# Kernel tuning notes

Measured on AMD Instinct MI355X. Metric: run time of the kernel, lower is better.

The kernel has to match this reference:

```python
import jax, jax.numpy as jnp
import numpy as np

N, D_IN = 8192, 1024
FC1, FC2, FC3 = 256, 128, 64
DQK = FC3 // 8  # 8


def setup_inputs() -> dict:
    key = jax.random.key(0)
    ks = jax.random.split(key, 20)
    s = 0.05
    inp = {
        "x": jax.random.normal(ks[0], (N, D_IN), jnp.float32),
        # feature extractor MLP (dropout omitted: eval mode)
        "W1": jax.random.normal(ks[1], (D_IN, FC1), jnp.float32) * s,
        "b1": jnp.zeros((FC1,), jnp.float32),
        "W2": jax.random.normal(ks[2], (FC1, FC2), jnp.float32) * s,
        "b2": jnp.zeros((FC2,), jnp.float32),
        "W3": jax.random.normal(ks[3], (FC2, FC3), jnp.float32) * s,
        "b3": jnp.zeros((FC3,), jnp.float32),
        # 1x1 conv Q/K/V == linear layers on the 64-dim embedding
        "Wq": jax.random.normal(ks[4], (FC3, DQK), jnp.float32) * s,
        "bq": jnp.zeros((DQK,), jnp.float32),
        "Wk": jax.random.normal(ks[5], (FC3, DQK), jnp.float32) * s,
        "bk": jnp.zeros((DQK,), jnp.float32),
        "Wv": jax.random.normal(ks[6], (FC3, FC3), jnp.float32) * s,
        "bv": jnp.zeros((FC3,), jnp.float32),
        "gamma": jnp.array([0.5], jnp.float32),  # learned residual scale (init 0 in torch)
        # attention-pooling branch
        "Wa1": jax.random.normal(ks[7], (FC3, FC3), jnp.float32) * s,
        "ba1": jnp.zeros((FC3,), jnp.float32),
        "Wa2": jax.random.normal(ks[8], (FC3, 1), jnp.float32) * s,
        "ba2": jnp.zeros((1,), jnp.float32),
        # classifier
        "Wc": jax.random.normal(ks[9], (FC3, 1), jnp.float32) * s,
        "bc": jnp.zeros((1,), jnp.float32),
    }
    return inp


def reference(x, W1, b1, W2, b2, W3, b3, Wq, bq, Wk, bk, Wv, bv, gamma,
              Wa1, ba1, Wa2, ba2, Wc, bc):
    # instance feature extractor (dropout identity at eval)
    H = jax.nn.relu(x @ W1 + b1)
    H = jax.nn.relu(H @ W2 + b2)
    H = jax.nn.relu(H @ W3 + b3)                 # [N, 64]
    # self-attention over instances (unscaled dot product)
    Q = H @ Wq + bq                              # [N, 8]
    K = H @ Wk + bk                              # [N, 8]
    V = H @ Wv + bv                              # [N, 64]
    att = jax.nn.softmax(Q @ K.T, axis=-1)       # [N, N] full score matrix
    H = gamma[0] * (att @ V) + H                 # residual scale-add
    # attention-based MIL pooling
    scores = jnp.tanh(H @ Wa1 + ba1) @ Wa2 + ba2 # [N, 1]
    A = jax.nn.softmax(scores[:, 0])             # [N]
    M = A @ H                                    # [64] bag embedding
    Y = jax.nn.sigmoid(M @ Wc + bc)[0]
    Y_prob = jnp.clip(Y, 1e-5, 1.0 - 1e-5)
    return (Y_prob, M)
```

## Files before the change

kernel.cpp:

```cpp
#include <hip/hip_runtime.h>
#include <math.h>

typedef unsigned short ushort_t;
typedef __attribute__((ext_vector_type(8))) short short8;
typedef __attribute__((ext_vector_type(4))) float f32x4;

__device__ inline unsigned bfpair(float lo, float hi) {
  unsigned r;
  asm("v_cvt_pk_bf16_f32 %0, %1, %2" : "=v"(r) : "v"(lo), "v"(hi));
  return r;
}
__device__ inline ushort_t bf16of(float v) { return (ushort_t)(bfpair(v, v) & 0xffffu); }
__device__ inline void permswap32(unsigned &a, unsigned &b) {
  asm("v_permlane32_swap_b32 %0, %1" : "+v"(a), "+v"(b));
}
__device__ inline void permswap16(unsigned &a, unsigned &b) {
  asm("v_permlane16_swap_b32 %0, %1" : "+v"(a), "+v"(b));
}

__device__ void transpose_tile(const float* __restrict__ W, ushort_t* __restrict__ Wt,
                               int K, int N, int bx, int by, int t)
{
  __shared__ float Ls[32][33];
  const int n0 = bx * 32, k0 = by * 32;
  const int tx = t & 31, tyb = t >> 5;
  #pragma unroll
  for (int s = 0; s < 4; ++s) {
    const int k = tyb + s * 8;
    Ls[k][tx] = W[(size_t)(k0 + k) * N + n0 + tx];
  }
  __syncthreads();
  #pragma unroll
  for (int s = 0; s < 2; ++s) {
    const int idx = t + 256 * s;
    const int n = idx >> 4, kk = (idx & 15) * 2;
    const unsigned pk = bfpair(Ls[kk][n], Ls[kk + 1][n]);
    *(unsigned*)&Wt[(size_t)(n0 + n) * K + k0 + kk] = pk;
  }
}

__global__ __launch_bounds__(256) void prep_all_k(
    const float* __restrict__ W1, ushort_t* __restrict__ W1t,
    const float* __restrict__ W2, ushort_t* __restrict__ W2t,
    const float* __restrict__ W3, ushort_t* __restrict__ W3t,
    const float* __restrict__ Wa1, ushort_t* __restrict__ Wa1t,
    const float* __restrict__ Wq, const float* __restrict__ Wk,
    const float* __restrict__ Wv, ushort_t* __restrict__ WqkvT)
{
  const int bid = blockIdx.x;
  const int t = threadIdx.x;
  if (bid < 256)      { transpose_tile(W1, W1t, 1024, 256, bid & 7, bid >> 3, t); }
  else if (bid < 288) { const int l = bid - 256; transpose_tile(W2, W2t, 256, 128, l & 3, l >> 2, t); }
  else if (bid < 296) { const int l = bid - 288; transpose_tile(W3, W3t, 128,  64, l & 1, l >> 1, t); }
  else if (bid < 300) { const int l = bid - 296; transpose_tile(Wa1, Wa1t, 64,  64, l & 1, l >> 1, t); }
  else {
    for (int e = t; e < 80 * 64; e += 256) {
      const int j = e >> 6, k = e & 63;
      float v;
      if (j < 8)       v = Wq[k * 8 + j];
      else if (j < 16) v = Wk[k * 8 + (j - 8)];
      else             v = Wv[k * 64 + (j - 16)];
      WqkvT[e] = bf16of(v);
    }
  }
}

__global__ __launch_bounds__(512) void gemm1_k(
    const float* __restrict__ Af, const ushort_t* __restrict__ Wt,
    const float* __restrict__ bias, ushort_t* __restrict__ C0)
{
  constexpr int K = 1024, N = 256, NK = K / 32;
  const int tid = threadIdx.x;
  const int wave = tid >> 6, lane = tid & 63;
  const int ln = lane & 15, g = lane >> 4;
  const int bm0 = blockIdx.x * 16;

  __shared__ ushort_t Als[2][16][40];
  __shared__ ushort_t Bls[2][N][40];

  const bool hasA = (tid < 64);
  const int arow = tid >> 2, akq = tid & 3;
  const int brow0 = tid >> 2, bkq0 = tid & 3;
  const int brow1 = (tid + 512) >> 2, bkq1 = (tid + 512) & 3;

  float4 rf0, rf1;
  short8 rb0, rb1;

  auto LOADK = [&](int ks) {
    const int k0 = ks * 32;
    if (hasA) {
      const float* src = &Af[(size_t)(bm0 + arow) * K + k0 + akq * 8];
      rf0 = *(const float4*)src;
      rf1 = *(const float4*)(src + 4);
    }
    rb0 = *(const short8*)&Wt[(size_t)brow0 * K + k0 + bkq0 * 8];
    rb1 = *(const short8*)&Wt[(size_t)brow1 * K + k0 + bkq1 * 8];
  };
  auto WRITEK = [&](int cur) {
    if (hasA) {
      union { unsigned u[4]; short8 s8; } cv;
      cv.u[0] = bfpair(rf0.x, rf0.y);
      cv.u[1] = bfpair(rf0.z, rf0.w);
      cv.u[2] = bfpair(rf1.x, rf1.y);
      cv.u[3] = bfpair(rf1.z, rf1.w);
      *(short8*)&Als[cur][arow][akq * 8] = cv.s8;
    }
    *(short8*)&Bls[cur][brow0][bkq0 * 8] = rb0;
    *(short8*)&Bls[cur][brow1][bkq1 * 8] = rb1;
  };

  f32x4 acc0 = {0.f, 0.f, 0.f, 0.f};
  f32x4 acc1 = {0.f, 0.f, 0.f, 0.f};

  LOADK(0);
  int cur = 0;
  for (int ks = 0; ks < NK; ++ks) {
    WRITEK(cur);
    __syncthreads();
    if (ks + 1 < NK) LOADK(ks + 1);
    const short8 af = *(const short8*)&Als[cur][ln][g * 8];
    const short8 b0 = *(const short8*)&Bls[cur][wave * 32 + ln][g * 8];
    const short8 b1 = *(const short8*)&Bls[cur][wave * 32 + 16 + ln][g * 8];
    acc0 = __builtin_amdgcn_mfma_f32_16x16x32_bf16(af, b0, acc0, 0, 0, 0);
    acc1 = __builtin_amdgcn_mfma_f32_16x16x32_bf16(af, b1, acc1, 0, 0, 0);
    cur ^= 1;
  }

  #pragma unroll
  for (int nt = 0; nt < 2; ++nt) {
    const f32x4 a = nt ? acc1 : acc0;
    #pragma unroll
    for (int r = 0; r < 4; ++r) {
      const int m = bm0 + 4 * g + r;
      const int n = wave * 32 + nt * 16 + ln;
      C0[(size_t)m * N + n] = bf16of(fmaxf(a[r] + bias[n], 0.f));
    }
  }
}

__global__ __launch_bounds__(256) void mlp23_qkv_k(
    const ushort_t* __restrict__ H1b, const ushort_t* __restrict__ W2t,
    const float* __restrict__ b2, const ushort_t* __restrict__ W3t,
    const float* __restrict__ b3, const ushort_t* __restrict__ WqkvT,
    const float* __restrict__ bq, const float* __restrict__ bk, const float* __restrict__ bv,
    float* __restrict__ H3, ushort_t* __restrict__ Qb, ushort_t* __restrict__ Kb,
    ushort_t* __restrict__ VT)
{
  const int wave = threadIdx.x >> 6, lane = threadIdx.x & 63;
  const int ln = lane & 15, g = lane >> 4;
  const int q0 = blockIdx.x * 16;
  const f32x4 zero4 = {0.f, 0.f, 0.f, 0.f};

  __shared__ ushort_t H2ls[16][136];
  __shared__ ushort_t Hls[16][72];

  f32x4 a2[2] = {zero4, zero4};
  #pragma unroll 2
  for (int k0 = 0; k0 < 256; k0 += 32) {
    const short8 af = *(const short8*)&H1b[(size_t)(q0 + ln) * 256 + k0 + g * 8];
    const short8 b0 = *(const short8*)&W2t[(size_t)(wave * 32 + ln) * 256 + k0 + g * 8];
    const short8 b1 = *(const short8*)&W2t[(size_t)(wave * 32 + 16 + ln) * 256 + k0 + g * 8];
    a2[0] = __builtin_amdgcn_mfma_f32_16x16x32_bf16(af, b0, a2[0], 0, 0, 0);
    a2[1] = __builtin_amdgcn_mfma_f32_16x16x32_bf16(af, b1, a2[1], 0, 0, 0);
  }
  #pragma unroll
  for (int nt = 0; nt < 2; ++nt)
    #pragma unroll
    for (int r = 0; r < 4; ++r) {
      const int n = wave * 32 + nt * 16 + ln;
      H2ls[4 * g + r][n] = bf16of(fmaxf(a2[nt][r] + b2[n], 0.f));
    }
  __syncthreads();

  f32x4 a3 = zero4;
  #pragma unroll
  for (int k0 = 0; k0 < 128; k0 += 32) {
    const short8 af = *(const short8*)&H2ls[ln][k0 + g * 8];
    const short8 bfr = *(const short8*)&W3t[(size_t)(wave * 16 + ln) * 128 + k0 + g * 8];
    a3 = __builtin_amdgcn_mfma_f32_16x16x32_bf16(af, bfr, a3, 0, 0, 0);
  }
  #pragma unroll
  for (int r = 0; r < 4; ++r) {
    const int m = q0 + 4 * g + r;
    const int n = wave * 16 + ln;
    float v = fmaxf(a3[r] + b3[n], 0.f);
    H3[(size_t)m * 64 + n] = v;
    Hls[4 * g + r][n] = bf16of(v);
  }
  __syncthreads();

  const int ntA = (wave == 0) ? 0 : (wave + 1);
  f32x4 accA = zero4, accB = zero4;
  #pragma unroll
  for (int k0 = 0; k0 < 64; k0 += 32) {
    const short8 af = *(const short8*)&Hls[ln][k0 + g * 8];
    const short8 bA = *(const short8*)&WqkvT[(size_t)(ntA * 16 + ln) * 64 + k0 + g * 8];
    accA = __builtin_amdgcn_mfma_f32_16x16x32_bf16(af, bA, accA, 0, 0, 0);
    if (wave == 0) {
      const short8 bB = *(const short8*)&WqkvT[(size_t)(16 + ln) * 64 + k0 + g * 8];
      accB = __builtin_amdgcn_mfma_f32_16x16x32_bf16(af, bB, accB, 0, 0, 0);
    }
  }
  if (wave == 0) {
    const float b0 = (ln < 8) ? bq[ln] : bk[ln - 8];
    #pragma unroll
    for (int r = 0; r < 4; ++r) {
      const int m = q0 + 4 * g + r;
      const float v = accA[r] + b0;
      if (ln < 8) Qb[(size_t)m * 8 + ln] = bf16of(v);
      else        Kb[(size_t)m * 8 + (ln - 8)] = bf16of(v);
    }
    const int d = ln;
    const float bb = bv[d];
    uint2 o;
    o.x = bfpair(accB[0] + bb, accB[1] + bb);
    o.y = bfpair(accB[2] + bb, accB[3] + bb);
    *(uint2*)&VT[(size_t)d * 8192 + q0 + 4 * g] = o;
  } else {
    const int d = (ntA - 1) * 16 + ln;
    const float bb = bv[d];
    uint2 o;
    o.x = bfpair(accA[0] + bb, accA[1] + bb);
    o.y = bfpair(accA[2] + bb, accA[3] + bb);
    *(uint2*)&VT[(size_t)d * 8192 + q0 + 4 * g] = o;
  }
}

__global__ __launch_bounds__(1024) void attn_part_k(
    const ushort_t* __restrict__ Qb, const ushort_t* __restrict__ Kb,
    const ushort_t* __restrict__ VT, float* __restrict__ Pnum,
    float* __restrict__ Pden)
{
  const int tid = threadIdx.x;
  const int wave = tid >> 6, lane = tid & 63;
  const int m = lane & 15, g = lane >> 4;
  const int qg = blockIdx.x & 31, js = blockIdx.x >> 5;
  const int q0 = qg * 256 + wave * 16;
  const int j0 = js * 1024;
  const f32x4 zero4 = {0.f,0.f,0.f,0.f};

  __shared__ ushort_t Vls[2][64][136];
  __shared__ ushort_t Kls[2][128][12];

  const int vd = tid >> 4, vc = tid & 15;
  const bool isK = (tid < 128);

  short8 vreg = {0,0,0,0,0,0,0,0}, kreg = {0,0,0,0,0,0,0,0};
  auto LOAD = [&](int jb) {
    vreg = *(const short8*)&VT[(size_t)vd * 8192 + jb + vc * 8];
    if (isK) kreg = *(const short8*)&Kb[(size_t)(jb + tid) * 8];
  };
  auto WRITE = [&](int cur) {
    *(short8*)&Vls[cur][vd][vc * 8] = vreg;
    if (isK) *(short8*)&Kls[cur][tid][0] = kreg;
  };

  short8 qf = {0,0,0,0,0,0,0,0};
  if (lane < 16) qf = *(const short8*)&Qb[(size_t)(q0 + m) * 8];

  f32x4 acc[4];
  #pragma unroll
  for (int dt=0;dt<4;dt++) acc[dt] = zero4;
  float lsum = 0.f;

  LOAD(j0);
  int cur = 0;
  for (int it = 0; it < 8; ++it) {
    WRITE(cur);
    __syncthreads();
    if (it + 1 < 8) LOAD(j0 + (it + 1) * 128);

    #pragma unroll
    for (int half = 0; half < 4; ++half) {
      short8 kf0 = {0,0,0,0,0,0,0,0}, kf1 = {0,0,0,0,0,0,0,0};
      if (lane < 16) {
        kf0 = *(const short8*)&Kls[cur][half*32 + m][0];
        kf1 = *(const short8*)&Kls[cur][half*32 + 16 + m][0];
      }
      const f32x4 s0 = __builtin_amdgcn_mfma_f32_16x16x32_bf16(kf0, qf, zero4, 0,0,0);
      const f32x4 s1 = __builtin_amdgcn_mfma_f32_16x16x32_bf16(kf1, qf, zero4, 0,0,0);
      const float e00 = __expf(s0[0]), e01 = __expf(s0[1]), e02 = __expf(s0[2]), e03 = __expf(s0[3]);
      const float e10 = __expf(s1[0]), e11 = __expf(s1[1]), e12 = __expf(s1[2]), e13 = __expf(s1[3]);
      lsum += ((e00+e01)+(e02+e03)) + ((e10+e11)+(e12+e13));
      unsigned X01 = bfpair(e00,e01), X23 = bfpair(e02,e03);
      unsigned Y01 = bfpair(e10,e11), Y23 = bfpair(e12,e13);
      permswap32(X01, Y01); permswap16(X01, Y01);
      permswap32(X23, Y23); permswap16(X23, Y23);
      union { unsigned u[4]; short8 s; } pfu;
      pfu.u[0] = X01;
      pfu.u[1] = X23;
      pfu.u[2] = Y01;
      pfu.u[3] = Y23;
      #pragma unroll
      for (int dt=0;dt<4;dt++) {
        const short8 vf = *(const short8*)&Vls[cur][dt*16 + m][half*32 + g * 8];
        acc[dt] = __builtin_amdgcn_mfma_f32_16x16x32_bf16(pfu.s, vf, acc[dt], 0,0,0);
      }
    }
    cur ^= 1;
  }

  lsum += __shfl_xor(lsum, 16, 64);
  lsum += __shfl_xor(lsum, 32, 64);

  float* np = &Pnum[((size_t)blockIdx.x * 256 + wave * 16) * 64];
  #pragma unroll
  for (int dt=0;dt<4;dt++)
    #pragma unroll
    for (int r=0;r<4;r++)
      np[(size_t)(4*g + r) * 64 + dt*16 + m] = acc[dt][r];
  if (lane < 16)
    Pden[(size_t)blockIdx.x * 256 + wave * 16 + m] = lsum;
}

__global__ __launch_bounds__(256) void epilogue_k(
    const float* __restrict__ Pnum, const float* __restrict__ Pden,
    const float* __restrict__ H3, const float* __restrict__ gamma,
    const ushort_t* __restrict__ Wa1t, const float* __restrict__ ba1,
    const float* __restrict__ Wa2, const float* __restrict__ ba2,
    float* __restrict__ pM, float* __restrict__ pS)
{
  const int wave = threadIdx.x >> 6, lane = threadIdx.x & 63;
  const int ln = lane & 15, g = lane >> 4;
  const int e = blockIdx.x;
  const int sub = e >> 5, qg = e & 31;
  const int q0 = qg * 256 + sub * 16;
  const f32x4 zero4 = {0.f, 0.f, 0.f, 0.f};

  __shared__ float Hals[16][68];
  __shared__ ushort_t Habls[16][72];
  __shared__ float scls[16];
  __shared__ float Ms[4][64];
  __shared__ float Ss[4];

  const float gm = gamma[0];
  #pragma unroll
  for (int rr = 0; rr < 4; ++rr) {
    const int r = wave * 4 + rr;
    const int q = q0 + r;
    const int qloc = q & 255;
    float num = 0.f, den = 0.f;
    #pragma unroll
    for (int js = 0; js < 8; ++js) {
      const size_t base = (size_t)(js * 32 + qg) * 256 + qloc;
      num += Pnum[base * 64 + lane];
      den += Pden[base];
    }
    const float hv = fmaf(gm, num / den, H3[(size_t)q * 64 + lane]);
    Hals[r][lane] = hv;
    Habls[r][lane] = bf16of(hv);
  }
  __syncthreads();

  f32x4 acc[4];
  #pragma unroll
  for (int nt = 0; nt < 4; ++nt) acc[nt] = zero4;
  #pragma unroll
  for (int k0 = 0; k0 < 64; k0 += 32) {
    const short8 af = *(const short8*)&Habls[ln][k0 + g * 8];
    #pragma unroll
    for (int nt = 0; nt < 4; ++nt) {
      const short8 bfr = *(const short8*)&Wa1t[(size_t)(nt * 16 + ln) * 64 + k0 + g * 8];
      acc[nt] = __builtin_amdgcn_mfma_f32_16x16x32_bf16(af, bfr, acc[nt], 0, 0, 0);
    }
  }
  #pragma unroll
  for (int r = 0; r < 4; ++r) {
    float s = 0.f;
    #pragma unroll
    for (int nt = 0; nt < 4; ++nt) {
      const int n = nt * 16 + ln;
      s += tanhf(acc[nt][r] + ba1[n]) * Wa2[n];
    }
    s += __shfl_xor(s, 1, 64); s += __shfl_xor(s, 2, 64);
    s += __shfl_xor(s, 4, 64); s += __shfl_xor(s, 8, 64);
    if (ln == 0) scls[4 * g + r] = s + ba2[0];
  }
  float macc = 0.f, se = 0.f;
  #pragma unroll
  for (int rr = 0; rr < 4; ++rr) {
    const int r = wave * 4 + rr;
    const float ee = __expf(scls[r]);
    se += ee;
    macc = fmaf(ee, Hals[r][lane], macc);
  }
  Ms[wave][lane] = macc;
  if (lane == 0) Ss[wave] = se;
  __syncthreads();
  if (wave == 0) {
    pM[(size_t)e * 64 + lane] = Ms[0][lane] + Ms[1][lane] + Ms[2][lane] + Ms[3][lane];
    if (lane == 0) pS[e] = Ss[0] + Ss[1] + Ss[2] + Ss[3];
  }
}

__global__ __launch_bounds__(1024) void pool2_k(
    const float* __restrict__ pM, const float* __restrict__ pS,
    const float* __restrict__ Wc, const float* __restrict__ bc,
    float* __restrict__ out)
{
  const int wave = threadIdx.x >> 6, lane = threadIdx.x & 63;
  __shared__ float Ms2[16][64];
  __shared__ float Ss2[16];
  float m_ = 0.f;
  #pragma unroll
  for (int i = 0; i < 32; ++i)
    m_ += pM[(size_t)(wave * 32 + i) * 64 + lane];
  Ms2[wave][lane] = m_;
  float s_ = (lane < 32) ? pS[wave * 32 + lane] : 0.f;
  s_ += __shfl_xor(s_, 1, 64);  s_ += __shfl_xor(s_, 2, 64);
  s_ += __shfl_xor(s_, 4, 64);  s_ += __shfl_xor(s_, 8, 64);
  s_ += __shfl_xor(s_, 16, 64); s_ += __shfl_xor(s_, 32, 64);
  if (lane == 0) Ss2[wave] = s_;
  __syncthreads();
  if (wave == 0) {
    float mm = 0.f, ss = 0.f;
    #pragma unroll
    for (int i = 0; i < 16; ++i) { mm += Ms2[i][lane]; ss += Ss2[i]; }
    const float Md = mm / ss;
    out[1 + lane] = Md;
    float yp = Md * Wc[lane];
    yp += __shfl_xor(yp, 1, 64);  yp += __shfl_xor(yp, 2, 64);
    yp += __shfl_xor(yp, 4, 64);  yp += __shfl_xor(yp, 8, 64);
    yp += __shfl_xor(yp, 16, 64); yp += __shfl_xor(yp, 32, 64);
    if (lane == 0) {
      float y = 1.f / (1.f + __expf(-(yp + bc[0])));
      y = fminf(fmaxf(y, 1e-5f), 1.f - 1e-5f);
      out[0] = y;
    }
  }
}

extern "C" void kernel_launch(void* const* d_in, const int* in_sizes, int n_in,
                              void* d_out, int out_size, void* d_ws, size_t ws_size,
                              hipStream_t stream)
{
  const float* x    = (const float*)d_in[0];
  const float* W1   = (const float*)d_in[1];
  const float* b1   = (const float*)d_in[2];
  const float* W2   = (const float*)d_in[3];
  const float* b2   = (const float*)d_in[4];
  const float* W3   = (const float*)d_in[5];
  const float* b3   = (const float*)d_in[6];
  const float* Wq   = (const float*)d_in[7];
  const float* bq   = (const float*)d_in[8];
  const float* Wk   = (const float*)d_in[9];
  const float* bk   = (const float*)d_in[10];
  const float* Wv   = (const float*)d_in[11];
  const float* bv   = (const float*)d_in[12];
  const float* gam  = (const float*)d_in[13];
  const float* Wa1  = (const float*)d_in[14];
  const float* ba1  = (const float*)d_in[15];
  const float* Wa2  = (const float*)d_in[16];
  const float* ba2  = (const float*)d_in[17];
  const float* Wc   = (const float*)d_in[18];
  const float* bc   = (const float*)d_in[19];
  float* out = (float*)d_out;

  char* w = (char*)d_ws;
  float* H3 = (float*)w;        w += (size_t)8192*64*4;
  float* pM = (float*)w;        w += 512*64*4;
  float* pS = (float*)w;        w += 512*4;
  float* Pnum = (float*)w;      w += (size_t)256*256*64*4;
  float* Pden = (float*)w;      w += (size_t)256*256*4;
  ushort_t* H1b = (ushort_t*)w; w += (size_t)8192*256*2;
  ushort_t* Qb  = (ushort_t*)w; w += (size_t)8192*8*2;
  ushort_t* Kb  = (ushort_t*)w; w += (size_t)8192*8*2;
  ushort_t* VT  = (ushort_t*)w; w += (size_t)64*8192*2;
  ushort_t* W1t = (ushort_t*)w; w += (size_t)256*1024*2;
  ushort_t* W2t = (ushort_t*)w; w += (size_t)128*256*2;
  ushort_t* W3t = (ushort_t*)w; w += (size_t)64*128*2;
  ushort_t* Wa1t= (ushort_t*)w; w += (size_t)64*64*2;
  ushort_t* Wqkv= (ushort_t*)w; w += (size_t)80*64*2;

  prep_all_k<<<301, 256, 0, stream>>>(W1, W1t, W2, W2t, W3, W3t, Wa1, Wa1t,
                                      Wq, Wk, Wv, Wqkv);
  gemm1_k<<<512, 512, 0, stream>>>(x, W1t, b1, H1b);
  mlp23_qkv_k<<<512, 256, 0, stream>>>(H1b, W2t, b2, W3t, b3, Wqkv,
                                       bq, bk, bv, H3, Qb, Kb, VT);
  attn_part_k<<<256, 1024, 0, stream>>>(Qb, Kb, VT, Pnum, Pden);
  epilogue_k<<<512, 256, 0, stream>>>(Pnum, Pden, H3, gam, Wa1t, ba1, Wa2, ba2, pM, pS);
  pool2_k<<<1, 1024, 0, stream>>>(pM, pS, Wc, bc, out);
}
```

Before: 76.17 us.

## Retile first GEMM to 64x64 blocks with direct global-to-LDS B loads

The first MLP GEMM moves from 16-row blocks spanning all 256 output columns to a 2D grid of 64x64 tiles. Each wave now computes a 2x2 set of MFMA tiles, which gives more register-level reuse of the A and B fragments. The weight tile is streamed into shared memory with global_load_lds instead of passing through registers, and the double-buffer schedule is reordered so there is one barrier per k-step. The trade-off is that each x row is now read and converted by four column-blocks instead of one, which raises the fp32 x traffic.

```diff
diff --git a/kernel.cpp b/kernel.cpp
--- a/kernel.cpp
+++ b/kernel.cpp
@@ -65,7 +65,7 @@
   }
 }
 
-__global__ __launch_bounds__(512) void gemm1_k(
+__global__ __launch_bounds__(256) void gemm1_k(
     const float* __restrict__ Af, const ushort_t* __restrict__ Wt,
     const float* __restrict__ bias, ushort_t* __restrict__ C0)
 {
@@ -73,69 +73,77 @@
   const int tid = threadIdx.x;
   const int wave = tid >> 6, lane = tid & 63;
   const int ln = lane & 15, g = lane >> 4;
-  const int bm0 = blockIdx.x * 16;
-
-  __shared__ ushort_t Als[2][16][40];
-  __shared__ ushort_t Bls[2][N][40];
-
-  const bool hasA = (tid < 64);
+  const int wm = wave >> 1, wn = wave & 1;
+  const int bm0 = blockIdx.x * 64;
+  const int bn0 = blockIdx.y * 64;
+
+  __shared__ ushort_t Als[2][64][32];
+  __shared__ ushort_t Bls[2][64][32];
+
   const int arow = tid >> 2, akq = tid & 3;
-  const int brow0 = tid >> 2, bkq0 = tid & 3;
-  const int brow1 = (tid + 512) >> 2, bkq1 = (tid + 512) & 3;
+  const ushort_t* bsrc = &Wt[(size_t)(bn0 + wave * 16 + (lane >> 2)) * K + (lane & 3) * 8];
 
   float4 rf0, rf1;
-  short8 rb0, rb1;
-
-  auto LOADK = [&](int ks) {
-    const int k0 = ks * 32;
-    if (hasA) {
-      const float* src = &Af[(size_t)(bm0 + arow) * K + k0 + akq * 8];
-      rf0 = *(const float4*)src;
-      rf1 = *(const float4*)(src + 4);
-    }
-    rb0 = *(const short8*)&Wt[(size_t)brow0 * K + k0 + bkq0 * 8];
-    rb1 = *(const short8*)&Wt[(size_t)brow1 * K + k0 + bkq1 * 8];
+  auto LOADA = [&](int ks) {
+    const float* src = &Af[(size_t)(bm0 + arow) * K + ks * 32 + akq * 8];
+    rf0 = *(const float4*)src;
+    rf1 = *(const float4*)(src + 4);
   };
-  auto WRITEK = [&](int cur) {
-    if (hasA) {
-      union { unsigned u[4]; short8 s8; } cv;
-      cv.u[0] = bfpair(rf0.x, rf0.y);
-      cv.u[1] = bfpair(rf0.z, rf0.w);
-      cv.u[2] = bfpair(rf1.x, rf1.y);
-      cv.u[3] = bfpair(rf1.z, rf1.w);
-      *(short8*)&Als[cur][arow][akq * 8] = cv.s8;
-    }
-    *(short8*)&Bls[cur][brow0][bkq0 * 8] = rb0;
-    *(short8*)&Bls[cur][brow1][bkq1 * 8] = rb1;
+  auto WRITEA = [&](int cur) {
+    union { unsigned u[4]; short8 s8; } cv;
+    cv.u[0] = bfpair(rf0.x, rf0.y);
+    cv.u[1] = bfpair(rf0.z, rf0.w);
+    cv.u[2] = bfpair(rf1.x, rf1.y);
+    cv.u[3] = bfpair(rf1.z, rf1.w);
+    *(short8*)&Als[cur][arow][akq * 8] = cv.s8;
   };
-
-  f32x4 acc0 = {0.f, 0.f, 0.f, 0.f};
-  f32x4 acc1 = {0.f, 0.f, 0.f, 0.f};
-
-  LOADK(0);
+  auto LOADB = [&](int ks, int cur) {
+    __builtin_amdgcn_global_load_lds(
+        (const __attribute__((address_space(1))) unsigned int*)(bsrc + ks * 32),
+        (__attribute__((address_space(3))) unsigned int*)&Bls[cur][wave * 16][0],
+        16, 0, 0);
+  };
+
+  f32x4 acc[2][2];
+  #pragma unroll
+  for (int mt = 0; mt < 2; ++mt)
+    #pragma unroll
+    for (int nt = 0; nt < 2; ++nt) acc[mt][nt] = (f32x4){0.f, 0.f, 0.f, 0.f};
+
+  LOADB(0, 0);
+  LOADA(0);
+  WRITEA(0);
+  __syncthreads();
   int cur = 0;
   for (int ks = 0; ks < NK; ++ks) {
-    WRITEK(cur);
+    if (ks + 1 < NK) { LOADB(ks + 1, cur ^ 1); LOADA(ks + 1); }
+    short8 af[2], bfr[2];
+    #pragma unroll
+    for (int mt = 0; mt < 2; ++mt)
+      af[mt] = *(const short8*)&Als[cur][wm * 32 + mt * 16 + ln][g * 8];
+    #pragma unroll
+    for (int nt = 0; nt < 2; ++nt)
+      bfr[nt] = *(const short8*)&Bls[cur][wn * 32 + nt * 16 + ln][g * 8];
+    #pragma unroll
+    for (int mt = 0; mt < 2; ++mt)
+      #pragma unroll
+      for (int nt = 0; nt < 2; ++nt)
+        acc[mt][nt] = __builtin_amdgcn_mfma_f32_16x16x32_bf16(af[mt], bfr[nt], acc[mt][nt], 0, 0, 0);
+    if (ks + 1 < NK) WRITEA(cur ^ 1);
     __syncthreads();
-    if (ks + 1 < NK) LOADK(ks + 1);
-    const short8 af = *(const short8*)&Als[cur][ln][g * 8];
-    const short8 b0 = *(const short8*)&Bls[cur][wave * 32 + ln][g * 8];
-    const short8 b1 = *(const short8*)&Bls[cur][wave * 32 + 16 + ln][g * 8];
-    acc0 = __builtin_amdgcn_mfma_f32_16x16x32_bf16(af, b0, acc0, 0, 0, 0);
-    acc1 = __builtin_amdgcn_mfma_f32_16x16x32_bf16(af, b1, acc1, 0, 0, 0);
     cur ^= 1;
   }
 
   #pragma unroll
-  for (int nt = 0; nt < 2; ++nt) {
-    const f32x4 a = nt ? acc1 : acc0;
-    #pragma unroll
-    for (int r = 0; r < 4; ++r) {
-      const int m = bm0 + 4 * g + r;
-      const int n = wave * 32 + nt * 16 + ln;
-      C0[(size_t)m * N + n] = bf16of(fmaxf(a[r] + bias[n], 0.f));
-    }
-  }
+  for (int mt = 0; mt < 2; ++mt)
+    #pragma unroll
+    for (int nt = 0; nt < 2; ++nt)
+      #pragma unroll
+      for (int r = 0; r < 4; ++r) {
+        const int m = bm0 + wm * 32 + mt * 16 + 4 * g + r;
+        const int n = bn0 + wn * 32 + nt * 16 + ln;
+        C0[(size_t)m * N + n] = bf16of(fmaxf(acc[mt][nt][r] + bias[n], 0.f));
+      }
 }
 
 __global__ __launch_bounds__(256) void mlp23_qkv_k(
@@ -474,7 +482,7 @@
 
   prep_all_k<<<301, 256, 0, stream>>>(W1, W1t, W2, W2t, W3, W3t, Wa1, Wa1t,
                                       Wq, Wk, Wv, Wqkv);
-  gemm1_k<<<512, 512, 0, stream>>>(x, W1t, b1, H1b);
+  gemm1_k<<<dim3(128, 4), 256, 0, stream>>>(x, W1t, b1, H1b);
   mlp23_qkv_k<<<512, 256, 0, stream>>>(H1b, W2t, b2, W3t, b3, Wqkv,
                                        bq, bk, bv, H3, Qb, Kb, VT);
   attn_part_k<<<256, 1024, 0, stream>>>(Qb, Kb, VT, Pnum, Pden);
```

New measurement: 74.36 us. 1.02x faster.
